# Performance work log

Measured on AMD Instinct MI355X. Metric: run time of the kernel, lower is better.

## Reference

```python
import jax, jax.numpy as jnp
import numpy as np

B, S, D, H = 2, 2048, 4096, 32
HD = D // H
FF = 22016 // 2  # QWenMLP gets intermediate_size // 2 = 11008
EPS = 1e-6
THETA = 10000.0


def setup_inputs() -> dict:
    key = jax.random.key(0)
    ks = jax.random.split(key, 10)
    s = lambda fan_in: 1.0 / np.sqrt(fan_in)
    return {
        "positions": jnp.broadcast_to(jnp.arange(S, dtype=jnp.int32), (B, S)),
        "hidden_states": jax.random.normal(ks[0], (B, S, D), jnp.float32),
        "ln1_w": jnp.ones((D,), jnp.float32),
        "ln2_w": jnp.ones((D,), jnp.float32),
        "Wqkv": jax.random.normal(ks[1], (D, 3 * D), jnp.float32) * s(D),
        "bqkv": jax.random.normal(ks[2], (3 * D,), jnp.float32) * 0.02,
        "Wo": jax.random.normal(ks[3], (D, D), jnp.float32) * s(D),
        "W1": jax.random.normal(ks[4], (D, FF), jnp.float32) * s(D),
        "W2": jax.random.normal(ks[5], (D, FF), jnp.float32) * s(D),
        "Wout": jax.random.normal(ks[6], (FF, D), jnp.float32) * s(FF),
    }


def _rmsnorm(x, w, eps=EPS):
    return x * jax.lax.rsqrt(jnp.mean(x * x, axis=-1, keepdims=True) + eps) * w


def _rope(x, positions):
    # x: [B, S, H, HD]; NeoX-style rotate-half RoPE over full head_dim
    inv_freq = 1.0 / (THETA ** (jnp.arange(0, HD, 2, dtype=jnp.float32) / HD))
    freqs = positions.astype(jnp.float32)[..., None] * inv_freq  # [B, S, HD/2]
    cos = jnp.concatenate([jnp.cos(freqs)] * 2, axis=-1)[:, :, None, :]
    sin = jnp.concatenate([jnp.sin(freqs)] * 2, axis=-1)[:, :, None, :]
    x1, x2 = jnp.split(x, 2, axis=-1)
    rotated = jnp.concatenate([-x2, x1], axis=-1)
    return x * cos + rotated * sin


def reference(positions, hidden_states, ln1_w, ln2_w, Wqkv, bqkv, Wo, W1, W2, Wout):
    residual = hidden_states
    h = _rmsnorm(hidden_states, ln1_w)
    qkv = h @ Wqkv + bqkv                              # [B, S, 3D]
    q, k, v = jnp.split(qkv, 3, axis=-1)
    q = _rope(q.reshape(B, S, H, HD), positions)
    k = _rope(k.reshape(B, S, H, HD), positions)
    v = v.reshape(B, S, H, HD)
    scores = jnp.einsum("bqhd,bkhd->bhqk", q, k) * (HD ** -0.5)
    causal = jnp.tril(jnp.ones((S, S), bool))
    scores = jnp.where(causal, scores, jnp.finfo(scores.dtype).min)
    probs = jax.nn.softmax(scores, axis=-1)
    attn = jnp.einsum("bhqk,bkhd->bqhd", probs, v).reshape(B, S, D)
    h = residual + attn @ Wo
    residual = h
    h = _rmsnorm(h, ln2_w)
    h = (h @ W1) * jax.nn.silu(h @ W2)                  # SwiGLU: w1(x) * silu(w2(x))
    return residual + h @ Wout
```

## Files before the change

kernel.cpp:

```cpp
#include <hip/hip_runtime.h>

typedef unsigned short u16;
typedef unsigned int   u32;
typedef __bf16 bf16x8 __attribute__((ext_vector_type(8)));
typedef float  f32x4  __attribute__((ext_vector_type(4)));
typedef unsigned short u16x4 __attribute__((ext_vector_type(4)));
typedef unsigned short u16x8 __attribute__((ext_vector_type(8)));

#define DEV __device__ __forceinline__

DEV u16 f2b(float f) {
  u32 u = __builtin_bit_cast(u32, f);
  return (u16)((u + 0x7fffu + ((u >> 16) & 1u)) >> 16);
}
DEV float b2f(u16 h) { u32 u = ((u32)h) << 16; return __builtin_bit_cast(float, u); }

DEV void gload16(const void* g, void* l) {
  __builtin_amdgcn_global_load_lds((__attribute__((address_space(1))) void*)(g),
                                   (__attribute__((address_space(3))) void*)(l),
                                   16, 0, 0);
}

DEV f32x4 MFMA(bf16x8 a, bf16x8 b, f32x4 c) {
  return __builtin_amdgcn_mfma_f32_16x16x32_bf16(a, b, c, 0, 0, 0);
}

__global__ __launch_bounds__(256) void transpose_cvt(const float* __restrict__ W,
                                                     u16* __restrict__ Wt,
                                                     int K, int N) {
  __shared__ float tile[32][33];
  const int n0 = blockIdx.x * 32, k0 = blockIdx.y * 32;
  const int tx = threadIdx.x, ty = threadIdx.y;
#pragma unroll
  for (int i = 0; i < 32; i += 8)
    tile[ty + i][tx] = W[(size_t)(k0 + ty + i) * N + n0 + tx];
  __syncthreads();
#pragma unroll
  for (int i = 0; i < 32; i += 8)
    Wt[(size_t)(n0 + ty + i) * K + k0 + tx] = f2b(tile[tx][ty + i]);
}

__global__ __launch_bounds__(256) void rmsnorm_k(const float* __restrict__ x,
                                                 const float* __restrict__ w,
                                                 u16* __restrict__ o, int D) {
  const int row = blockIdx.x, tid = threadIdx.x;
  const float4* xr = (const float4*)(x + (size_t)row * D);
  const float4* wr = (const float4*)w;
  float4 v[4];
  float ss = 0.f;
#pragma unroll
  for (int i = 0; i < 4; ++i) {
    v[i] = xr[i * 256 + tid];
    ss += v[i].x * v[i].x + v[i].y * v[i].y + v[i].z * v[i].z + v[i].w * v[i].w;
  }
#pragma unroll
  for (int off = 1; off < 64; off <<= 1) ss += __shfl_xor(ss, off, 64);
  __shared__ float red[4];
  if ((tid & 63) == 0) red[tid >> 6] = ss;
  __syncthreads();
  const float tot = red[0] + red[1] + red[2] + red[3];
  const float sc = rsqrtf(tot / (float)D + 1e-6f);
  u16x4* orow = (u16x4*)(o + (size_t)row * D);
#pragma unroll
  for (int i = 0; i < 4; ++i) {
    float4 wv = wr[i * 256 + tid];
    u16x4 p;
    p[0] = f2b(v[i].x * sc * wv.x);
    p[1] = f2b(v[i].y * sc * wv.y);
    p[2] = f2b(v[i].z * sc * wv.z);
    p[3] = f2b(v[i].w * sc * wv.w);
    orow[i * 256 + tid] = p;
  }
}

__global__ __launch_bounds__(256) void rope_table(const int* __restrict__ positions,
                                                  float* __restrict__ tab, int BS) {
  const int idx = blockIdx.x * 256 + threadIdx.x;
  if (idx >= BS * 64) return;
  const int bs = idx >> 6, i = idx & 63;
  const float pos = (float)positions[bs];
  const float inv = __expf(-(float)i * (9.210340371976184f / 64.f));
  const float ang = pos * inv;
  float s, c;
  sincosf(ang, &s, &c);
  tab[idx] = c;
  tab[BS * 64 + idx] = s;
}

__global__ __launch_bounds__(256) void rope_apply(u16* __restrict__ qkv,
                                                  const float* __restrict__ tab, int BS) {
  const int idx = blockIdx.x * 256 + threadIdx.x;
  if (idx >= BS * 2048) return;
  const int i = idx & 63, h = (idx >> 6) & 31, bs = idx >> 11;
  const float c = tab[bs * 64 + i];
  const float s = tab[(size_t)BS * 64 + bs * 64 + i];
  const size_t base = (size_t)bs * 12288 + h * 128 + i;
  float x1 = b2f(qkv[base]), x2 = b2f(qkv[base + 64]);
  qkv[base] = f2b(x1 * c - x2 * s);
  qkv[base + 64] = f2b(x2 * c + x1 * s);
  float y1 = b2f(qkv[base + 4096]), y2 = b2f(qkv[base + 4096 + 64]);
  qkv[base + 4096] = f2b(y1 * c - y2 * s);
  qkv[base + 4096 + 64] = f2b(y2 * c + y1 * s);
}

template <int MODE>
__global__ __launch_bounds__(512, 2) void gemm256(const u16* __restrict__ A,
                                                  const u16* __restrict__ Bt,
                                                  void* __restrict__ outp,
                                                  const float* __restrict__ bias,
                                                  const float* __restrict__ resid,
                                                  const u16* __restrict__ g1,
                                                  int M, int N, int K) {
  __shared__ __align__(16) u16 As0[256 * 64], As1[256 * 64];
  __shared__ __align__(16) u16 Bs0[256 * 64], Bs1[256 * 64];
  const int tid = threadIdx.x;
  const int wid = tid >> 6, l = tid & 63;
  const int wm = wid >> 2, wn = wid & 3;
  const int lr = l & 15, lc = l >> 4;
  const int gx = gridDim.x;
  const int nwg = gx * gridDim.y;
  const int orig = blockIdx.y * gx + blockIdx.x;
  const int wg = (orig & 7) * (nwg >> 3) + (orig >> 3);
  const int m0 = (wg / gx) * 256, n0 = (wg % gx) * 256;

  const int NT = K >> 6;
  const int srow = wid * 8 + (l >> 3);
  const int scol = (l & 7) * 8;
  const u16* Ag = A + (size_t)(m0 + srow) * K + scol;
  const u16* Bg = Bt + (size_t)(n0 + srow) * K + scol;

  f32x4 acc[8][4] = {};

  auto STAGE = [&](u16* asn, u16* bsn, int k0) {
#pragma unroll
    for (int c = 0; c < 4; ++c) {
      gload16(Ag + (size_t)(c * 64) * K + k0, asn + (c * 64 + wid * 8) * 64);
      gload16(Bg + (size_t)(c * 64) * K + k0, bsn + (c * 64 + wid * 8) * 64);
    }
  };

  auto ITER = [&](int t, const u16* as, const u16* bs, u16* asn, u16* bsn) {
    asm volatile("s_barrier" ::: "memory");
    if (t + 1 < NT) {
      STAGE(asn, bsn, (t + 1) << 6);
      asm volatile("s_waitcnt vmcnt(8)" ::: "memory");
    } else {
      asm volatile("s_waitcnt vmcnt(0)" ::: "memory");
    }
    asm volatile("s_barrier" ::: "memory");
    bf16x8 bfr[4][2];
#pragma unroll
    for (int nf = 0; nf < 4; ++nf) {
      bfr[nf][0] = *(const bf16x8*)&bs[(wn * 64 + nf * 16 + lr) * 64 + lc * 8];
      bfr[nf][1] = *(const bf16x8*)&bs[(wn * 64 + nf * 16 + lr) * 64 + 32 + lc * 8];
    }
    __builtin_amdgcn_s_setprio(1);
#pragma unroll
    for (int mf = 0; mf < 8; ++mf) {
      const bf16x8 af0 = *(const bf16x8*)&as[(wm * 128 + mf * 16 + lr) * 64 + lc * 8];
      const bf16x8 af1 = *(const bf16x8*)&as[(wm * 128 + mf * 16 + lr) * 64 + 32 + lc * 8];
#pragma unroll
      for (int nf = 0; nf < 4; ++nf) {
        acc[mf][nf] = MFMA(af0, bfr[nf][0], acc[mf][nf]);
        acc[mf][nf] = MFMA(af1, bfr[nf][1], acc[mf][nf]);
      }
    }
    __builtin_amdgcn_s_setprio(0);
  };

  STAGE(As0, Bs0, 0);
  for (int t = 0; t < NT; t += 2) {
    ITER(t,     As0, Bs0, As1, Bs1);
    ITER(t + 1, As1, Bs1, As0, Bs0);
  }

#pragma unroll
  for (int mf = 0; mf < 8; ++mf) {
#pragma unroll
    for (int nf = 0; nf < 4; ++nf) {
      const int gr = m0 + wm * 128 + mf * 16 + lc * 4;
      const int gc = n0 + wn * 64 + nf * 16 + lr;
#pragma unroll
      for (int r = 0; r < 4; ++r) {
        float v = acc[mf][nf][r];
        const size_t idx = (size_t)(gr + r) * N + gc;
        if constexpr (MODE == 0) {
          ((u16*)outp)[idx] = f2b(v);
        } else if constexpr (MODE == 1) {
          ((u16*)outp)[idx] = f2b(v + bias[gc]);
        } else if constexpr (MODE == 2) {
          ((float*)outp)[idx] = v + resid[idx];
        } else {
          const float g = b2f(g1[idx]);
          const float sv = v / (1.f + __expf(-v));
          ((u16*)outp)[idx] = f2b(g * sv);
        }
      }
    }
  }
}

__global__ __launch_bounds__(256) void attn_kernel(const u16* __restrict__ qkv,
                                                   u16* __restrict__ o, int S) {
  const int qtile = gridDim.x - 1 - blockIdx.x;
  const int bh = blockIdx.y;
  const int b = bh >> 5, h = bh & 31;
  const int q0 = qtile * 64;
  const int tid = threadIdx.x;
  const int w = tid >> 6, l = tid & 63;
  const int lr = l & 15, lc = l >> 4;
  const size_t RS = 12288;
  const float SCALE = 0.08838834764831845f;

  __shared__ __align__(16) u16 Ks[64 * 128];
  __shared__ __align__(16) u16 Vt[128 * 64];
  __shared__ __align__(16) u16 Ps[4][16 * 64];

  bf16x8 qf[4];
  {
    const u16* qp = qkv + (size_t)(b * S + q0 + w * 16 + lr) * RS + h * 128 + 8 * lc;
#pragma unroll
    for (int kc = 0; kc < 4; ++kc) qf[kc] = *(const bf16x8*)(qp + kc * 32);
  }

  float m_[4], ls[4];
  f32x4 O[8] = {};
#pragma unroll
  for (int r = 0; r < 4; ++r) { m_[r] = -3e38f; ls[r] = 0.f; }

  const int nkt = qtile + 1;
  for (int kt = 0; kt < nkt; ++kt) {
    const int k0 = kt * 64;
#pragma unroll
    for (int it = 0; it < 4; ++it) {
      const int eid = it * 256 + tid;
      const int kr = eid >> 4, d0 = (eid & 15) * 8;
      u16x8 k8 = *(const u16x8*)(qkv + (size_t)(b * S + k0 + kr) * RS + 4096 + h * 128 + d0);
      *(u16x8*)&Ks[kr * 128 + (d0 ^ ((kr & 7) * 8))] = k8;
    }
#pragma unroll
    for (int it = 0; it < 4; ++it) {
      const int d0 = (it * 4 + w) * 8;
      u16x8 v8 = *(const u16x8*)(qkv + (size_t)(b * S + k0 + l) * RS + 8192 + h * 128 + d0);
#pragma unroll
      for (int jj = 0; jj < 8; ++jj) {
        const int d = d0 + jj;
        Vt[(d * 64 + l) ^ ((d & 7) * 8)] = v8[jj];
      }
    }
    __syncthreads();

    const int nks = (kt == qtile) ? (w + 1) : 4;
    float sv[4][4];
#pragma unroll
    for (int ks = 0; ks < 4; ++ks) {
      if (ks < nks) {
        const int row = ks * 16 + lr;
        f32x4 sacc = {0.f, 0.f, 0.f, 0.f};
#pragma unroll
        for (int kc = 0; kc < 4; ++kc) {
          bf16x8 kf = *(const bf16x8*)&Ks[row * 128 + ((kc * 32 + 8 * lc) ^ ((lr & 7) * 8))];
          sacc = MFMA(qf[kc], kf, sacc);
        }
        const bool dm = (kt == qtile) && (ks == w);
#pragma unroll
        for (int r = 0; r < 4; ++r) {
          float x = sacc[r] * SCALE;
          if (dm) {
            const int kg = ks * 16 + lr, qg = w * 16 + lc * 4 + r;
            if (kg > qg) x = -3e38f;
          }
          sv[ks][r] = x;
        }
      } else {
#pragma unroll
        for (int r = 0; r < 4; ++r) sv[ks][r] = -3e38f;
      }
    }

    float alpha[4];
#pragma unroll
    for (int r = 0; r < 4; ++r) {
      float pm = fmaxf(fmaxf(sv[0][r], sv[1][r]), fmaxf(sv[2][r], sv[3][r]));
#pragma unroll
      for (int off = 1; off < 16; off <<= 1) pm = fmaxf(pm, __shfl_xor(pm, off, 64));
      const float mn = fmaxf(m_[r], pm);
      alpha[r] = __expf(m_[r] - mn);
      m_[r] = mn;
    }
    float p[4][4];
#pragma unroll
    for (int ks = 0; ks < 4; ++ks)
#pragma unroll
      for (int r = 0; r < 4; ++r) {
        p[ks][r] = __expf(sv[ks][r] - m_[r]);
        const int q = lc * 4 + r, k = ks * 16 + lr;
        Ps[w][q * 64 + (k ^ ((q & 7) * 8))] = f2b(p[ks][r]);
      }
#pragma unroll
    for (int r = 0; r < 4; ++r) {
      float s = p[0][r] + p[1][r] + p[2][r] + p[3][r];
#pragma unroll
      for (int off = 1; off < 16; off <<= 1) s += __shfl_xor(s, off, 64);
      ls[r] = ls[r] * alpha[r] + s;
    }
#pragma unroll
    for (int dt = 0; dt < 8; ++dt)
#pragma unroll
      for (int r = 0; r < 4; ++r) O[dt][r] *= alpha[r];

#pragma unroll
    for (int half = 0; half < 2; ++half) {
      const bf16x8 ap = *(const bf16x8*)&Ps[w][lr * 64 + ((half * 32 + 8 * lc) ^ ((lr & 7) * 8))];
#pragma unroll
      for (int dt = 0; dt < 8; ++dt) {
        const int d = dt * 16 + lr;
        const bf16x8 bv = *(const bf16x8*)&Vt[d * 64 + ((half * 32 + 8 * lc) ^ ((d & 7) * 8))];
        O[dt] = MFMA(ap, bv, O[dt]);
      }
    }
    __syncthreads();
  }

  float inv[4];
#pragma unroll
  for (int r = 0; r < 4; ++r) inv[r] = 1.f / ls[r];
#pragma unroll
  for (int dt = 0; dt < 8; ++dt)
#pragma unroll
    for (int r = 0; r < 4; ++r) {
      const int qg = q0 + w * 16 + lc * 4 + r;
      o[(size_t)(b * S + qg) * 4096 + h * 128 + dt * 16 + lr] = f2b(O[dt][r] * inv[r]);
    }
}

extern "C" void kernel_launch(void* const* d_in, const int* in_sizes, int n_in,
                              void* d_out, int out_size, void* d_ws, size_t ws_size,
                              hipStream_t stream) {
  const int*   positions = (const int*)d_in[0];
  const float* hidden    = (const float*)d_in[1];
  const float* ln1       = (const float*)d_in[2];
  const float* ln2       = (const float*)d_in[3];
  const float* Wqkv      = (const float*)d_in[4];
  const float* bqkv      = (const float*)d_in[5];
  const float* Wo        = (const float*)d_in[6];
  const float* W1        = (const float*)d_in[7];
  const float* W2        = (const float*)d_in[8];
  const float* Wout      = (const float*)d_in[9];
  float* out = (float*)d_out;

  const int S = 2048, BS = 4096, D = 4096, FF = 11008, N3 = 12288;

  char* ws = (char*)d_ws;
  size_t off = 0;
  auto alloc = [&](size_t bytes) { void* p = ws + off; off += (bytes + 255) & ~(size_t)255; return p; };
  u16*   WT    = (u16*)alloc((size_t)N3 * D * 2);
  u16*   qkv   = (u16*)alloc((size_t)BS * N3 * 2);
  u16*   slotH = (u16*)alloc((size_t)BS * D * 2);
  float* h2    = (float*)alloc((size_t)BS * D * 4);
  u16*   slotG = (u16*)alloc((size_t)BS * FF * 2);
  float* tab   = (float*)alloc((size_t)2 * BS * 64 * 4);
  if (ws_size < off) return;

  rope_table<<<(BS * 64 + 255) / 256, 256, 0, stream>>>(positions, tab, BS);

  transpose_cvt<<<dim3(N3 / 32, D / 32), dim3(32, 8), 0, stream>>>(Wqkv, WT, D, N3);
  rmsnorm_k<<<BS, 256, 0, stream>>>(hidden, ln1, slotH, D);
  gemm256<1><<<dim3(N3 / 256, BS / 256), 512, 0, stream>>>(slotH, WT, qkv, bqkv, nullptr, nullptr, BS, N3, D);
  rope_apply<<<(BS * 2048) / 256, 256, 0, stream>>>(qkv, tab, BS);

  attn_kernel<<<dim3(S / 64, 64), 256, 0, stream>>>(qkv, slotH, S);

  transpose_cvt<<<dim3(D / 32, D / 32), dim3(32, 8), 0, stream>>>(Wo, WT, D, D);
  gemm256<2><<<dim3(D / 256, BS / 256), 512, 0, stream>>>(slotH, WT, h2, nullptr, hidden, nullptr, BS, D, D);

  rmsnorm_k<<<BS, 256, 0, stream>>>(h2, ln2, slotH, D);
  transpose_cvt<<<dim3(FF / 32, D / 32), dim3(32, 8), 0, stream>>>(W1, WT, D, FF);
  gemm256<0><<<dim3(FF / 256, BS / 256), 512, 0, stream>>>(slotH, WT, slotG, nullptr, nullptr, nullptr, BS, FF, D);
  transpose_cvt<<<dim3(FF / 32, D / 32), dim3(32, 8), 0, stream>>>(W2, WT, D, FF);
  gemm256<3><<<dim3(FF / 256, BS / 256), 512, 0, stream>>>(slotH, WT, slotG, nullptr, nullptr, slotG, BS, FF, D);
  transpose_cvt<<<dim3(D / 32, FF / 32), dim3(32, 8), 0, stream>>>(Wout, WT, FF, D);
  gemm256<2><<<dim3(D / 256, BS / 256), 512, 0, stream>>>(slotG, WT, out, nullptr, h2, nullptr, BS, D, FF);
}
```

Measured before the change: 2.608 ms.

## Switch GEMM to three-stage BK=32 LDS pipeline with single barrier per step

```diff
diff --git a/kernel.cpp b/kernel.cpp
--- a/kernel.cpp
+++ b/kernel.cpp
@@ -104,15 +104,15 @@
 }
 
 template <int MODE>
-__global__ __launch_bounds__(512, 2) void gemm256(const u16* __restrict__ A,
+__global__ __launch_bounds__(512, 1) void gemm256(const u16* __restrict__ A,
                                                   const u16* __restrict__ Bt,
                                                   void* __restrict__ outp,
                                                   const float* __restrict__ bias,
                                                   const float* __restrict__ resid,
                                                   const u16* __restrict__ g1,
                                                   int M, int N, int K) {
-  __shared__ __align__(16) u16 As0[256 * 64], As1[256 * 64];
-  __shared__ __align__(16) u16 Bs0[256 * 64], Bs1[256 * 64];
+  __shared__ __align__(16) u16 As[3][256 * 32];
+  __shared__ __align__(16) u16 Bs[3][256 * 32];
   const int tid = threadIdx.x;
   const int wid = tid >> 6, l = tid & 63;
   const int wm = wid >> 2, wn = wid & 3;
@@ -123,55 +123,53 @@
   const int wg = (orig & 7) * (nwg >> 3) + (orig >> 3);
   const int m0 = (wg / gx) * 256, n0 = (wg % gx) * 256;
 
-  const int NT = K >> 6;
-  const int srow = wid * 8 + (l >> 3);
-  const int scol = (l & 7) * 8;
-  const u16* Ag = A + (size_t)(m0 + srow) * K + scol;
-  const u16* Bg = Bt + (size_t)(n0 + srow) * K + scol;
+  const int NT = K >> 5;
+  const u16* Ag = A + (size_t)(m0 + (tid >> 2)) * K + (tid & 3) * 8;
+  const u16* Bg = Bt + (size_t)(n0 + (tid >> 2)) * K + (tid & 3) * 8;
 
   f32x4 acc[8][4] = {};
 
-  auto STAGE = [&](u16* asn, u16* bsn, int k0) {
-#pragma unroll
-    for (int c = 0; c < 4; ++c) {
-      gload16(Ag + (size_t)(c * 64) * K + k0, asn + (c * 64 + wid * 8) * 64);
-      gload16(Bg + (size_t)(c * 64) * K + k0, bsn + (c * 64 + wid * 8) * 64);
-    }
+  auto STAGE = [&](int t, u16* da, u16* db) {
+    gload16(Ag + t * 32, da + tid * 8);
+    gload16(Ag + (size_t)128 * K + t * 32, da + 4096 + tid * 8);
+    gload16(Bg + t * 32, db + tid * 8);
+    gload16(Bg + (size_t)128 * K + t * 32, db + 4096 + tid * 8);
   };
 
-  auto ITER = [&](int t, const u16* as, const u16* bs, u16* asn, u16* bsn) {
-    asm volatile("s_barrier" ::: "memory");
+  auto BODY = [&](int t, const u16* ca, const u16* cb, u16* na, u16* nb) {
+    if (t + 2 < NT) STAGE(t + 2, na, nb);
+    bf16x8 bf[4];
+#pragma unroll
+    for (int nf = 0; nf < 4; ++nf)
+      bf[nf] = *(const bf16x8*)&cb[(wn * 64 + nf * 16 + lr) * 32 + lc * 8];
+    __builtin_amdgcn_s_setprio(1);
+#pragma unroll
+    for (int mf = 0; mf < 8; ++mf) {
+      const bf16x8 af = *(const bf16x8*)&ca[(wm * 128 + mf * 16 + lr) * 32 + lc * 8];
+#pragma unroll
+      for (int nf = 0; nf < 4; ++nf) acc[mf][nf] = MFMA(af, bf[nf], acc[mf][nf]);
+    }
+    __builtin_amdgcn_s_setprio(0);
+    if (t + 2 < NT) {
+      asm volatile("s_waitcnt vmcnt(4)" ::: "memory");
+    } else if (t + 1 < NT) {
+      asm volatile("s_waitcnt vmcnt(0)" ::: "memory");
+    }
     if (t + 1 < NT) {
-      STAGE(asn, bsn, (t + 1) << 6);
-      asm volatile("s_waitcnt vmcnt(8)" ::: "memory");
-    } else {
-      asm volatile("s_waitcnt vmcnt(0)" ::: "memory");
-    }
-    asm volatile("s_barrier" ::: "memory");
-    bf16x8 bfr[4][2];
-#pragma unroll
-    for (int nf = 0; nf < 4; ++nf) {
-      bfr[nf][0] = *(const bf16x8*)&bs[(wn * 64 + nf * 16 + lr) * 64 + lc * 8];
-      bfr[nf][1] = *(const bf16x8*)&bs[(wn * 64 + nf * 16 + lr) * 64 + 32 + lc * 8];
-    }
-    __builtin_amdgcn_s_setprio(1);
-#pragma unroll
-    for (int mf = 0; mf < 8; ++mf) {
-      const bf16x8 af0 = *(const bf16x8*)&as[(wm * 128 + mf * 16 + lr) * 64 + lc * 8];
-      const bf16x8 af1 = *(const bf16x8*)&as[(wm * 128 + mf * 16 + lr) * 64 + 32 + lc * 8];
-#pragma unroll
-      for (int nf = 0; nf < 4; ++nf) {
-        acc[mf][nf] = MFMA(af0, bfr[nf][0], acc[mf][nf]);
-        acc[mf][nf] = MFMA(af1, bfr[nf][1], acc[mf][nf]);
-      }
-    }
-    __builtin_amdgcn_s_setprio(0);
+      asm volatile("s_waitcnt lgkmcnt(0)" ::: "memory");
+      asm volatile("s_barrier" ::: "memory");
+    }
   };
 
-  STAGE(As0, Bs0, 0);
-  for (int t = 0; t < NT; t += 2) {
-    ITER(t,     As0, Bs0, As1, Bs1);
-    ITER(t + 1, As1, Bs1, As0, Bs0);
+  STAGE(0, As[0], Bs[0]);
+  STAGE(1, As[1], Bs[1]);
+  asm volatile("s_waitcnt vmcnt(4)" ::: "memory");
+  asm volatile("s_barrier" ::: "memory");
+
+  for (int t = 0; t < NT; t += 3) {
+    BODY(t, As[0], Bs[0], As[2], Bs[2]);
+    if (t + 1 < NT) BODY(t + 1, As[1], Bs[1], As[0], Bs[0]);
+    if (t + 2 < NT) BODY(t + 2, As[2], Bs[2], As[1], Bs[1]);
   }
 
 #pragma unroll
```

After: 2.534 ms. 1.03x faster.

## Restructure GEMM main loop into four half-K LDS buffers with XOR swizzle

Applied to the files above, without the earlier changes.

```diff
diff --git a/kernel.cpp b/kernel.cpp
--- a/kernel.cpp
+++ b/kernel.cpp
@@ -111,8 +111,8 @@
                                                   const float* __restrict__ resid,
                                                   const u16* __restrict__ g1,
                                                   int M, int N, int K) {
-  __shared__ __align__(16) u16 As0[256 * 64], As1[256 * 64];
-  __shared__ __align__(16) u16 Bs0[256 * 64], Bs1[256 * 64];
+  __shared__ __align__(16) u16 A0s[256 * 32], A1s[256 * 32];
+  __shared__ __align__(16) u16 B0s[256 * 32], B1s[256 * 32];
   const int tid = threadIdx.x;
   const int wid = tid >> 6, l = tid & 63;
   const int wm = wid >> 2, wn = wid & 3;
@@ -124,55 +124,91 @@
   const int m0 = (wg / gx) * 256, n0 = (wg % gx) * 256;
 
   const int NT = K >> 6;
-  const int srow = wid * 8 + (l >> 3);
-  const int scol = (l & 7) * 8;
-  const u16* Ag = A + (size_t)(m0 + srow) * K + scol;
-  const u16* Bg = Bt + (size_t)(n0 + srow) * K + scol;
+  const int rt = tid >> 2;
+  const int ct = (tid & 3) ^ (rt & 3);
+  const u16* aS = A + (size_t)(m0 + rt) * K + ct * 8;
+  const u16* bS = Bt + (size_t)(n0 + rt) * K + ct * 8;
+
+  auto STG = [&](u16* reg, const u16* src, int koff) {
+    gload16(src + koff, reg + wid * 512);
+    gload16(src + (size_t)128 * K + koff, reg + 4096 + wid * 512);
+  };
+  auto RA = [&](const u16* reg, int mf) {
+    const int r = wm * 128 + mf * 16 + lr;
+    return *(const bf16x8*)&reg[r * 32 + ((lc ^ (r & 3)) * 8)];
+  };
+  auto RB = [&](const u16* reg, int nf) {
+    const int r = wn * 64 + nf * 16 + lr;
+    return *(const bf16x8*)&reg[r * 32 + ((lc ^ (r & 3)) * 8)];
+  };
 
   f32x4 acc[8][4] = {};
 
-  auto STAGE = [&](u16* asn, u16* bsn, int k0) {
-#pragma unroll
-    for (int c = 0; c < 4; ++c) {
-      gload16(Ag + (size_t)(c * 64) * K + k0, asn + (c * 64 + wid * 8) * 64);
-      gload16(Bg + (size_t)(c * 64) * K + k0, bsn + (c * 64 + wid * 8) * 64);
-    }
-  };
-
-  auto ITER = [&](int t, const u16* as, const u16* bs, u16* asn, u16* bsn) {
-    asm volatile("s_barrier" ::: "memory");
-    if (t + 1 < NT) {
-      STAGE(asn, bsn, (t + 1) << 6);
-      asm volatile("s_waitcnt vmcnt(8)" ::: "memory");
-    } else {
-      asm volatile("s_waitcnt vmcnt(0)" ::: "memory");
-    }
-    asm volatile("s_barrier" ::: "memory");
-    bf16x8 bfr[4][2];
-#pragma unroll
-    for (int nf = 0; nf < 4; ++nf) {
-      bfr[nf][0] = *(const bf16x8*)&bs[(wn * 64 + nf * 16 + lr) * 64 + lc * 8];
-      bfr[nf][1] = *(const bf16x8*)&bs[(wn * 64 + nf * 16 + lr) * 64 + 32 + lc * 8];
-    }
+#define BAR() asm volatile("s_barrier" ::: "memory")
+#define VM2() asm volatile("s_waitcnt vmcnt(2)" ::: "memory")
+
+  STG(A0s, aS, 0);
+  STG(B0s, bS, 0);
+  STG(A1s, aS, 32);
+  VM2();
+  BAR();
+
+  for (int t = 0; t < NT; ++t) {
+    const int k0 = t << 6, k1 = (t + 1) << 6;
+    bf16x8 afr[8], bq0, bq1;
+#pragma unroll
+    for (int mf = 0; mf < 8; ++mf) afr[mf] = RA(A0s, mf);
+    bq0 = RB(B0s, 0); bq1 = RB(B0s, 1);
+    STG(B1s, bS, k0 + 32);
+    BAR();
     __builtin_amdgcn_s_setprio(1);
 #pragma unroll
     for (int mf = 0; mf < 8; ++mf) {
-      const bf16x8 af0 = *(const bf16x8*)&as[(wm * 128 + mf * 16 + lr) * 64 + lc * 8];
-      const bf16x8 af1 = *(const bf16x8*)&as[(wm * 128 + mf * 16 + lr) * 64 + 32 + lc * 8];
-#pragma unroll
-      for (int nf = 0; nf < 4; ++nf) {
-        acc[mf][nf] = MFMA(af0, bfr[nf][0], acc[mf][nf]);
-        acc[mf][nf] = MFMA(af1, bfr[nf][1], acc[mf][nf]);
-      }
+      acc[mf][0] = MFMA(afr[mf], bq0, acc[mf][0]);
+      acc[mf][1] = MFMA(afr[mf], bq1, acc[mf][1]);
     }
     __builtin_amdgcn_s_setprio(0);
-  };
-
-  STAGE(As0, Bs0, 0);
-  for (int t = 0; t < NT; t += 2) {
-    ITER(t,     As0, Bs0, As1, Bs1);
-    ITER(t + 1, As1, Bs1, As0, Bs0);
-  }
+    BAR();
+    bq0 = RB(B0s, 2); bq1 = RB(B0s, 3);
+    if (t + 1 < NT) STG(A0s, aS, k1);
+    BAR();
+    __builtin_amdgcn_s_setprio(1);
+#pragma unroll
+    for (int mf = 0; mf < 8; ++mf) {
+      acc[mf][2] = MFMA(afr[mf], bq0, acc[mf][2]);
+      acc[mf][3] = MFMA(afr[mf], bq1, acc[mf][3]);
+    }
+    __builtin_amdgcn_s_setprio(0);
+    VM2();
+    BAR();
+#pragma unroll
+    for (int mf = 0; mf < 8; ++mf) afr[mf] = RA(A1s, mf);
+    bq0 = RB(B1s, 0); bq1 = RB(B1s, 1);
+    if (t + 1 < NT) STG(B0s, bS, k1);
+    BAR();
+    __builtin_amdgcn_s_setprio(1);
+#pragma unroll
+    for (int mf = 0; mf < 8; ++mf) {
+      acc[mf][0] = MFMA(afr[mf], bq0, acc[mf][0]);
+      acc[mf][1] = MFMA(afr[mf], bq1, acc[mf][1]);
+    }
+    __builtin_amdgcn_s_setprio(0);
+    BAR();
+    bq0 = RB(B1s, 2); bq1 = RB(B1s, 3);
+    if (t + 1 < NT) STG(A1s, aS, k1 + 32);
+    BAR();
+    __builtin_amdgcn_s_setprio(1);
+#pragma unroll
+    for (int mf = 0; mf < 8; ++mf) {
+      acc[mf][2] = MFMA(afr[mf], bq0, acc[mf][2]);
+      acc[mf][3] = MFMA(afr[mf], bq1, acc[mf][3]);
+    }
+    __builtin_amdgcn_s_setprio(0);
+    VM2();
+    BAR();
+  }
+#undef BAR
+#undef VM2
 
 #pragma unroll
   for (int mf = 0; mf < 8; ++mf) {
```

New measurement: 2.474 ms. 5.1% less time.
